# Kernel optimization log

Measured on AMD Instinct MI355X. Metric: run time of the kernel, lower is better.

Reference implementation:

```python
import jax, jax.numpy as jnp
import numpy as np

N_EMBD = 1024
N_HEAD = 16

def setup_inputs() -> dict:
    key = jax.random.key(0)
    ks = jax.random.split(key, 5)
    C = N_EMBD
    x = jax.random.normal(ks[0], (4, 2048, C), dtype=jnp.float32)
    s = 1.0 / np.sqrt(C)
    W_attn = jax.random.normal(ks[1], (C, 3 * C), dtype=jnp.float32) * s
    b_attn = jnp.zeros((3 * C,), dtype=jnp.float32)
    W_proj = jax.random.normal(ks[2], (C, C), dtype=jnp.float32) * s
    b_proj = jnp.zeros((C,), dtype=jnp.float32)
    return {"x": x, "W_attn": W_attn, "b_attn": b_attn, "W_proj": W_proj, "b_proj": b_proj}

def reference(x, W_attn, b_attn, W_proj, b_proj):
    B, S, C = x.shape
    Nh = N_HEAD
    Ne = C // Nh
    qkv = x @ W_attn + b_attn                      # [B,S,3C]
    q, k, v = jnp.split(qkv, 3, axis=-1)
    def heads(t):
        return t.reshape(B, S, Nh, Ne).transpose(0, 2, 1, 3)  # [B,Nh,S,Ne]
    q, k, v = heads(q), heads(k), heads(v)
    scale = 1.0 / np.sqrt(Ne)
    att = scale * jnp.einsum('bhqe,bhke->bhqk', q, k)          # [B,Nh,S,S]
    mask = jnp.tril(jnp.ones((S, S), dtype=bool))
    att = jnp.where(mask, att, -jnp.inf)
    att = jax.nn.softmax(att, axis=-1)
    y = jnp.einsum('bhqk,bhke->bhqe', att, v)                  # [B,Nh,S,Ne]
    y = y.transpose(0, 2, 1, 3).reshape(B, S, C)
    return y @ W_proj + b_proj
```

## Files before the change

### kernel.cpp

```cpp
#include <hip/hip_runtime.h>
#include <cstdint>
#include <cstddef>

typedef _Float16 h16;
typedef _Float16 h16x4 __attribute__((ext_vector_type(4)));
typedef _Float16 h16x8 __attribute__((ext_vector_type(8)));
typedef __fp16 fp16x2 __attribute__((ext_vector_type(2)));
typedef float f32x4 __attribute__((ext_vector_type(4)));

#define LOG2E 1.44269504088896f
#define QSCALE (0.125f * LOG2E)
#define THR 11.0f

static __device__ __forceinline__ f32x4 mfma_f16(h16x8 a, h16x8 b, f32x4 c) {
  return __builtin_amdgcn_mfma_f32_16x16x32_f16(a, b, c, 0, 0, 0);
}

static __device__ __forceinline__ void gload_lds16(const void* g, void* s) {
  __builtin_amdgcn_global_load_lds(
      (__attribute__((address_space(1))) void*)(uintptr_t)g,
      (__attribute__((address_space(3))) void*)s, 16, 0, 0);
}

__global__ __launch_bounds__(256) void k_cvt(const float* __restrict__ in,
                                             h16* __restrict__ out, int n) {
  int i = (blockIdx.x * 256 + threadIdx.x) * 8;
  if (i >= n) return;
  float4 a = *(const float4*)(in + i);
  float4 b = *(const float4*)(in + i + 4);
  h16x8 o;
  o[0] = (h16)a.x; o[1] = (h16)a.y; o[2] = (h16)a.z; o[3] = (h16)a.w;
  o[4] = (h16)b.x; o[5] = (h16)b.y; o[6] = (h16)b.z; o[7] = (h16)b.w;
  *(h16x8*)(out + i) = o;
}

__global__ __launch_bounds__(256) void k_tr_cvt(const float* __restrict__ in,
                                                h16* __restrict__ out, int R, int C) {
  __shared__ float tile[32][33];
  int c0 = blockIdx.x * 32, r0 = blockIdx.y * 32;
  int tx = threadIdx.x & 31, ty = threadIdx.x >> 5;
#pragma unroll
  for (int i = 0; i < 4; i++) {
    int r = ty + i * 8;
    tile[r][tx] = in[(size_t)(r0 + r) * C + c0 + tx];
  }
  __syncthreads();
#pragma unroll
  for (int i = 0; i < 4; i++) {
    int c = ty + i * 8;
    out[(size_t)(c0 + c) * R + r0 + tx] = (h16)tile[tx][c];
  }
}

static __device__ __forceinline__ void gemm_main(const h16* __restrict__ A,
                                                 const h16* __restrict__ BT,
                                                 int K, int m0, int n0,
                                                 h16* sA, h16* sB, f32x4 acc[4][4]) {
  const int t = threadIdx.x;
  const int l = t & 63, w = t >> 6;
  const int lm = l & 15, lh = l >> 4;
  const int wm = (w >> 1) * 64, wn = (w & 1) * 64;

  const h16* gA0 = A + (size_t)(m0 + (t >> 2)) * K + (t & 3) * 8;
  const h16* gB0 = BT + (size_t)(n0 + (t >> 2)) * K + (t & 3) * 8;
  h16* sAw = sA + w * 512;
  h16* sBw = sB + w * 512;

  for (int k0 = 0; k0 < K; k0 += 32) {
    gload_lds16(gA0 + k0, sAw);
    gload_lds16(gA0 + (size_t)64 * K + k0, sAw + 2048);
    gload_lds16(gB0 + k0, sBw);
    gload_lds16(gB0 + (size_t)64 * K + k0, sBw + 2048);
    __syncthreads();
    h16x8 af[4], bfv[4];
#pragma unroll
    for (int mi = 0; mi < 4; mi++)
      af[mi] = *(const h16x8*)(sA + (wm + mi * 16 + lm) * 32 + lh * 8);
#pragma unroll
    for (int ni = 0; ni < 4; ni++)
      bfv[ni] = *(const h16x8*)(sB + (wn + ni * 16 + lm) * 32 + lh * 8);
#pragma unroll
    for (int mi = 0; mi < 4; mi++)
#pragma unroll
      for (int ni = 0; ni < 4; ni++)
        acc[mi][ni] = mfma_f16(af[mi], bfv[ni], acc[mi][ni]);
    __syncthreads();
  }
}

__global__ __launch_bounds__(256) void k_gemm_qkv(const h16* __restrict__ xb,
                                                  const h16* __restrict__ WTa,
                                                  const float* __restrict__ b_attn,
                                                  h16* __restrict__ qb, h16* __restrict__ kbuf,
                                                  h16* __restrict__ vT) {
  __shared__ __align__(16) h16 sA[128 * 32];
  __shared__ __align__(16) h16 sB[128 * 32];
  f32x4 acc[4][4];
#pragma unroll
  for (int i = 0; i < 4; i++)
#pragma unroll
    for (int j = 0; j < 4; j++) acc[i][j] = (f32x4){0.f, 0.f, 0.f, 0.f};
  const int n0 = blockIdx.x * 128, m0 = blockIdx.y * 128;
  gemm_main(xb, WTa, 1024, m0, n0, sA, sB, acc);

  const int t = threadIdx.x, l = t & 63, w = t >> 6;
  const int lm = l & 15, lh = l >> 4;
  const int wm = (w >> 1) * 64, wn = (w & 1) * 64;
#pragma unroll
  for (int mi = 0; mi < 4; mi++) {
#pragma unroll
    for (int ni = 0; ni < 4; ni++) {
      const int n = n0 + wn + ni * 16 + lm;
      const float bias = b_attn[n];
      const int which = n >> 10, c = n & 1023, h = c >> 6, e = c & 63;
#pragma unroll
      for (int r = 0; r < 4; r++) {
        const int m = m0 + wm + mi * 16 + lh * 4 + r;
        const int b = m >> 11, s = m & 2047;
        const h16 o = (h16)(acc[mi][ni][r] + bias);
        const size_t bh = (size_t)(b * 16 + h);
        if (which == 0)      qb[(bh * 2048 + s) * 64 + e] = o;
        else if (which == 1) kbuf[(bh * 2048 + s) * 64 + e] = o;
        else                 vT[(bh * 64 + e) * 2048 + s] = o;
      }
    }
  }
}

__global__ __launch_bounds__(256) void k_gemm_proj(const h16* __restrict__ yb,
                                                   const h16* __restrict__ WTp,
                                                   const float* __restrict__ b_proj,
                                                   float* __restrict__ out) {
  __shared__ __align__(16) h16 sA[128 * 32];
  __shared__ __align__(16) h16 sB[128 * 32];
  f32x4 acc[4][4];
#pragma unroll
  for (int i = 0; i < 4; i++)
#pragma unroll
    for (int j = 0; j < 4; j++) acc[i][j] = (f32x4){0.f, 0.f, 0.f, 0.f};
  const int n0 = blockIdx.x * 128, m0 = blockIdx.y * 128;
  gemm_main(yb, WTp, 1024, m0, n0, sA, sB, acc);

  const int t = threadIdx.x, l = t & 63, w = t >> 6;
  const int lm = l & 15, lh = l >> 4;
  const int wm = (w >> 1) * 64, wn = (w & 1) * 64;
#pragma unroll
  for (int mi = 0; mi < 4; mi++) {
#pragma unroll
    for (int ni = 0; ni < 4; ni++) {
      const int n = n0 + wn + ni * 16 + lm;
      const float bias = b_proj[n];
#pragma unroll
      for (int r = 0; r < 4; r++) {
        const int m = m0 + wm + mi * 16 + lh * 4 + r;
        out[(size_t)m * 1024 + n] = acc[mi][ni][r] + bias;
      }
    }
  }
}

__global__ __launch_bounds__(256, 3) void k_attn(const h16* __restrict__ qb,
                                                 const h16* __restrict__ kbuf,
                                                 const h16* __restrict__ vT,
                                                 h16* __restrict__ yb) {
  __shared__ __align__(16) h16 sKt[2][64 * 64];
  __shared__ __align__(16) h16 sVt[2][64 * 64];
  __shared__ __align__(16) h16 sP[4][2][16 * 64];

  const int bid = blockIdx.x;
  const int bh = bid & 63;
  const int qt = 15 - (bid >> 6);
  const int b = bh >> 4, h = bh & 15;
  const int tid = threadIdx.x, lam = tid & 63, w = tid >> 6;
  const int lm = lam & 15, lh = lam >> 4;
  const int q0 = qt * 128 + w * 32;
  const h16* Q = qb + (size_t)bh * 2048 * 64;
  const h16* Kp = kbuf + (size_t)bh * 2048 * 64;
  const h16* Vp = vT + (size_t)bh * 64 * 2048;

  const int srow = lam >> 3;
  const int xo8 = (((lam & 7) ^ (srow & 7)) << 3);

  h16x8 qf[2][2];
#pragma unroll
  for (int rt = 0; rt < 2; rt++)
#pragma unroll
    for (int dc = 0; dc < 2; dc++) {
      h16x8 qv = *(const h16x8*)(Q + (size_t)(q0 + rt * 16 + lm) * 64 + dc * 32 + lh * 8);
      h16x8 o;
#pragma unroll
      for (int i = 0; i < 8; i++) o[i] = (h16)((float)qv[i] * QSCALE);
      qf[rt][dc] = o;
    }

  f32x4 yacc[2][4];
  float m2[2], lw[2];
#pragma unroll
  for (int rt = 0; rt < 2; rt++) {
    m2[rt] = -1e30f;
    lw[rt] = 0.f;
#pragma unroll
    for (int i = 0; i < 4; i++) yacc[rt][i] = (f32x4){0.f, 0.f, 0.f, 0.f};
  }

  const int nsteps = qt * 2 + 2;

#pragma unroll
  for (int i = 0; i < 2; i++) {
    const int seg = 2 * w + i;
    const int r = seg * 8 + srow;
    gload_lds16(Kp + (size_t)r * 64 + xo8, &sKt[0][seg * 512]);
    gload_lds16(Vp + (size_t)r * 2048 + xo8, &sVt[0][seg * 512]);
  }
  asm volatile("s_waitcnt vmcnt(0)" ::: "memory");
  __syncthreads();

  for (int tt = 0; tt < nsteps; ++tt) {
    const int kb0 = tt * 64, cur = tt & 1;
    if (tt + 1 < nsteps) {
      const int kn = kb0 + 64;
#pragma unroll
      for (int i = 0; i < 2; i++) {
        const int seg = 2 * w + i;
        const int r = seg * 8 + srow;
        gload_lds16(Kp + (size_t)(kn + r) * 64 + xo8, &sKt[cur ^ 1][seg * 512]);
        gload_lds16(Vp + (size_t)r * 2048 + kn + xo8, &sVt[cur ^ 1][seg * 512]);
      }
    }
    if (kb0 <= q0 + 31) {
      const bool domask = (kb0 + 63 > q0);
      h16x8 kf[4][2];
#pragma unroll
      for (int ct = 0; ct < 4; ct++)
#pragma unroll
        for (int dc = 0; dc < 2; dc++)
          kf[ct][dc] = *(const h16x8*)(
              &sKt[cur][(ct * 16 + lm) * 64 + ((dc * 32 + lh * 8) ^ ((lm & 7) << 3))]);
      h16x8 vf[4][2];
#pragma unroll
      for (int dt = 0; dt < 4; dt++)
#pragma unroll
        for (int kc = 0; kc < 2; kc++)
          vf[dt][kc] = *(const h16x8*)(
              &sVt[cur][(dt * 16 + lm) * 64 + ((kc * 32 + lh * 8) ^ ((lm & 7) << 3))]);

#pragma unroll
      for (int rt = 0; rt < 2; rt++) {
        const int qrow = q0 + rt * 16 + lm;
        f32x4 sv[4];
        __builtin_amdgcn_s_setprio(1);
#pragma unroll
        for (int ct = 0; ct < 4; ct++) {
          f32x4 s = mfma_f16(kf[ct][0], qf[rt][0], (f32x4){0.f, 0.f, 0.f, 0.f});
          sv[ct] = mfma_f16(kf[ct][1], qf[rt][1], s);
        }
        __builtin_amdgcn_s_setprio(0);
        if (domask) {
#pragma unroll
          for (int ct = 0; ct < 4; ct++)
#pragma unroll
            for (int r = 0; r < 4; r++)
              if (kb0 + ct * 16 + lh * 4 + r > qrow) sv[ct][r] = -1e30f;
        }
        float rm = fmaxf(fmaxf(fmaxf(sv[0][0], sv[0][1]), fmaxf(sv[0][2], sv[0][3])),
                         fmaxf(fmaxf(sv[1][0], sv[1][1]), fmaxf(sv[1][2], sv[1][3])));
        rm = fmaxf(rm, fmaxf(fmaxf(fmaxf(sv[2][0], sv[2][1]), fmaxf(sv[2][2], sv[2][3])),
                             fmaxf(fmaxf(sv[3][0], sv[3][1]), fmaxf(sv[3][2], sv[3][3]))));
        rm = fmaxf(rm, __shfl_xor(rm, 16));
        rm = fmaxf(rm, __shfl_xor(rm, 32));
        if (!__all(rm <= m2[rt] + THR)) {
          const float nm = fmaxf(m2[rt], rm);
          const float alpha = __builtin_amdgcn_exp2f(m2[rt] - nm);
          m2[rt] = nm;
          lw[rt] *= alpha;
#pragma unroll
          for (int dt = 0; dt < 4; dt++) yacc[rt][dt] *= alpha;
        }
        const float m = m2[rt];
        float psum = 0.f;
#pragma unroll
        for (int ct = 0; ct < 4; ct++) {
          const float p0 = __builtin_amdgcn_exp2f(sv[ct][0] - m);
          const float p1 = __builtin_amdgcn_exp2f(sv[ct][1] - m);
          const float p2 = __builtin_amdgcn_exp2f(sv[ct][2] - m);
          const float p3 = __builtin_amdgcn_exp2f(sv[ct][3] - m);
          psum += (p0 + p1) + (p2 + p3);
          const fp16x2 u0 = __builtin_amdgcn_cvt_pkrtz(p0, p1);
          const fp16x2 u1 = __builtin_amdgcn_cvt_pkrtz(p2, p3);
          const int base = ct * 16 + lh * 4;
          *(fp16x2*)(&sP[w][rt][lm * 64 + ((base + 0) ^ ((lm & 7) << 3))]) = u0;
          *(fp16x2*)(&sP[w][rt][lm * 64 + ((base + 2) ^ ((lm & 7) << 3))]) = u1;
        }
        lw[rt] += psum;
      }
#pragma unroll
      for (int rt = 0; rt < 2; rt++) {
        const h16x8 pf0 = *(const h16x8*)(
            &sP[w][rt][lm * 64 + ((lh * 8) ^ ((lm & 7) << 3))]);
        const h16x8 pf1 = *(const h16x8*)(
            &sP[w][rt][lm * 64 + ((32 + lh * 8) ^ ((lm & 7) << 3))]);
        __builtin_amdgcn_s_setprio(1);
#pragma unroll
        for (int dt = 0; dt < 4; dt++) {
          f32x4 y = mfma_f16(vf[dt][0], pf0, yacc[rt][dt]);
          yacc[rt][dt] = mfma_f16(vf[dt][1], pf1, y);
        }
        __builtin_amdgcn_s_setprio(0);
      }
    }
    asm volatile("s_waitcnt vmcnt(0)" ::: "memory");
    __syncthreads();
  }

#pragma unroll
  for (int rt = 0; rt < 2; rt++) {
    float s = lw[rt];
    s += __shfl_xor(s, 16);
    s += __shfl_xor(s, 32);
    const float inv = 1.0f / s;
    const int q = q0 + rt * 16 + lm;
    const size_t yrow = ((size_t)b * 2048 + q) * 1024 + h * 64;
#pragma unroll
    for (int dt = 0; dt < 4; dt++) {
      h16x4 o;
#pragma unroll
      for (int r = 0; r < 4; r++) o[r] = (h16)(yacc[rt][dt][r] * inv);
      *(h16x4*)(yb + yrow + dt * 16 + lh * 4) = o;
    }
  }
}

extern "C" void kernel_launch(void* const* d_in, const int* in_sizes, int n_in,
                              void* d_out, int out_size, void* d_ws, size_t ws_size,
                              hipStream_t stream) {
  const float* x      = (const float*)d_in[0];
  const float* W_attn = (const float*)d_in[1];
  const float* b_attn = (const float*)d_in[2];
  const float* W_proj = (const float*)d_in[3];
  const float* b_proj = (const float*)d_in[4];
  float* out = (float*)d_out;

  char* ws = (char*)d_ws;
  h16* xb   = (h16*)(ws);
  h16* WTa  = (h16*)(ws + 16777216);
  h16* WTp  = (h16*)(ws + 23068672);
  h16* qb   = (h16*)(ws + 25165824);
  h16* kbuf = (h16*)(ws + 41943040);
  h16* vT   = (h16*)(ws + 58720256);
  h16* yb   = xb;

  k_cvt<<<dim3(8192 * 1024 / 2048), 256, 0, stream>>>(x, xb, 8192 * 1024);
  k_tr_cvt<<<dim3(3072 / 32, 1024 / 32), 256, 0, stream>>>(W_attn, WTa, 1024, 3072);
  k_tr_cvt<<<dim3(1024 / 32, 1024 / 32), 256, 0, stream>>>(W_proj, WTp, 1024, 1024);
  k_gemm_qkv<<<dim3(3072 / 128, 8192 / 128), 256, 0, stream>>>(xb, WTa, b_attn, qb, kbuf, vT);
  k_attn<<<dim3(64 * 16), 256, 0, stream>>>(qb, kbuf, vT, yb);
  k_gemm_proj<<<dim3(1024 / 128, 8192 / 128), 256, 0, stream>>>(yb, WTp, b_proj, out);
}
```

Baseline: 299.5 us.

## Rewrite GEMMs with 256x128 tiles, triple-buffered async LDS loads, swizzle and XCD remap

Both projection GEMMs now use 512-thread blocks on 256x128 tiles with K-step 64. Loads go to a three-slot LDS ring through async global_load_lds, waited on with vmcnt and a single barrier per iteration, so two stages are in flight during compute. LDS columns are XOR-swizzled to avoid bank conflicts, and block IDs are remapped across the 8 XCDs for cache locality. The goal is to hide global latency and remove the two-barrier, single-buffer stalls of the old loop, at the cost of more LDS per block (144KB) and fewer resident blocks.

```diff
diff --git a/kernel.cpp b/kernel.cpp
--- a/kernel.cpp
+++ b/kernel.cpp
@@ -52,73 +52,108 @@
   }
 }
 
-static __device__ __forceinline__ void gemm_main(const h16* __restrict__ A,
-                                                 const h16* __restrict__ BT,
-                                                 int K, int m0, int n0,
-                                                 h16* sA, h16* sB, f32x4 acc[4][4]) {
-  const int t = threadIdx.x;
-  const int l = t & 63, w = t >> 6;
-  const int lm = l & 15, lh = l >> 4;
-  const int wm = (w >> 1) * 64, wn = (w & 1) * 64;
-
-  const h16* gA0 = A + (size_t)(m0 + (t >> 2)) * K + (t & 3) * 8;
-  const h16* gB0 = BT + (size_t)(n0 + (t >> 2)) * K + (t & 3) * 8;
-  h16* sAw = sA + w * 512;
-  h16* sBw = sB + w * 512;
-
-  for (int k0 = 0; k0 < K; k0 += 32) {
-    gload_lds16(gA0 + k0, sAw);
-    gload_lds16(gA0 + (size_t)64 * K + k0, sAw + 2048);
-    gload_lds16(gB0 + k0, sBw);
-    gload_lds16(gB0 + (size_t)64 * K + k0, sBw + 2048);
-    __syncthreads();
-    h16x8 af[4], bfv[4];
+#define SLOT_H16 24576
+#define NT_K 16
+
+static __device__ __forceinline__ void gemm_main256(
+    const h16* __restrict__ A, const h16* __restrict__ BT,
+    int m0, int n0, h16* sAB, f32x4 acc[4][4]) {
+  const int tid = threadIdx.x;
+  const int lane = tid & 63, w = tid >> 6;
+  const int lm = lane & 15, lh = lane >> 4;
+  const int wr = w >> 1, wc = w & 1;
+  const int wbase = w * 512;
+  const int srow = tid >> 3;
+  const int scol = (((tid & 7) ^ (srow & 7)) << 3);
+  const h16* gA = A + (size_t)(m0 + srow) * 1024 + scol;
+  const h16* gB = BT + (size_t)(n0 + srow) * 1024 + scol;
+
+  auto stage = [&](int t, int sl) {
+    const int k = t * 64;
+    h16* d = sAB + sl * SLOT_H16 + wbase;
+    gload_lds16(gA + (size_t)0 * 65536 + k, d + 0 * 4096);
+    gload_lds16(gA + (size_t)1 * 65536 + k, d + 1 * 4096);
+    gload_lds16(gA + (size_t)2 * 65536 + k, d + 2 * 4096);
+    gload_lds16(gA + (size_t)3 * 65536 + k, d + 3 * 4096);
+    gload_lds16(gB + (size_t)0 * 65536 + k, d + 16384 + 0 * 4096);
+    gload_lds16(gB + (size_t)1 * 65536 + k, d + 16384 + 1 * 4096);
+  };
+
+  stage(0, 0);
+  stage(1, 1);
+  asm volatile("s_waitcnt vmcnt(6)" ::: "memory");
+  __builtin_amdgcn_s_barrier();
+
+  int sl = 0, ss = 2;
+  for (int t = 0; t < NT_K; ++t) {
+    if (t < NT_K - 2) stage(t + 2, ss);
+    const h16* sa = sAB + sl * SLOT_H16;
+    const h16* sb = sa + 16384;
+    h16x8 af[4][2], bf[4][2];
+#pragma unroll
+    for (int mi = 0; mi < 4; mi++) {
+      const int row = wr * 64 + mi * 16 + lm;
+#pragma unroll
+      for (int kk = 0; kk < 2; kk++)
+        af[mi][kk] = *(const h16x8*)(sa + row * 64 + ((kk * 32 + lh * 8) ^ ((lm & 7) << 3)));
+    }
+#pragma unroll
+    for (int ni = 0; ni < 4; ni++) {
+      const int row = wc * 64 + ni * 16 + lm;
+#pragma unroll
+      for (int kk = 0; kk < 2; kk++)
+        bf[ni][kk] = *(const h16x8*)(sb + row * 64 + ((kk * 32 + lh * 8) ^ ((lm & 7) << 3)));
+    }
+    __builtin_amdgcn_s_setprio(1);
 #pragma unroll
     for (int mi = 0; mi < 4; mi++)
-      af[mi] = *(const h16x8*)(sA + (wm + mi * 16 + lm) * 32 + lh * 8);
-#pragma unroll
-    for (int ni = 0; ni < 4; ni++)
-      bfv[ni] = *(const h16x8*)(sB + (wn + ni * 16 + lm) * 32 + lh * 8);
-#pragma unroll
-    for (int mi = 0; mi < 4; mi++)
 #pragma unroll
       for (int ni = 0; ni < 4; ni++)
-        acc[mi][ni] = mfma_f16(af[mi], bfv[ni], acc[mi][ni]);
-    __syncthreads();
-  }
-}
-
-__global__ __launch_bounds__(256) void k_gemm_qkv(const h16* __restrict__ xb,
-                                                  const h16* __restrict__ WTa,
-                                                  const float* __restrict__ b_attn,
-                                                  h16* __restrict__ qb, h16* __restrict__ kbuf,
-                                                  h16* __restrict__ vT) {
-  __shared__ __align__(16) h16 sA[128 * 32];
-  __shared__ __align__(16) h16 sB[128 * 32];
+        acc[mi][ni] = mfma_f16(af[mi][1], bf[ni][1],
+                               mfma_f16(af[mi][0], bf[ni][0], acc[mi][ni]));
+    __builtin_amdgcn_s_setprio(0);
+    if (t < NT_K - 2) asm volatile("s_waitcnt vmcnt(6)" ::: "memory");
+    else              asm volatile("s_waitcnt vmcnt(0)" ::: "memory");
+    __builtin_amdgcn_s_barrier();
+    sl = (sl == 2) ? 0 : sl + 1;
+    ss = (ss == 2) ? 0 : ss + 1;
+  }
+}
+
+__global__ __launch_bounds__(512, 2) void k_gemm_qkv(const h16* __restrict__ xb,
+                                                     const h16* __restrict__ WTa,
+                                                     const float* __restrict__ b_attn,
+                                                     h16* __restrict__ qb,
+                                                     h16* __restrict__ kbuf,
+                                                     h16* __restrict__ vT) {
+  __shared__ __align__(16) h16 sAB[3 * SLOT_H16];
+  const int bid = blockIdx.x;
+  const int flat = (bid & 7) * 96 + (bid >> 3);
+  const int mt = flat / 24, nt = flat % 24;
+  const int m0 = mt * 256, n0 = nt * 128;
   f32x4 acc[4][4];
 #pragma unroll
   for (int i = 0; i < 4; i++)
 #pragma unroll
     for (int j = 0; j < 4; j++) acc[i][j] = (f32x4){0.f, 0.f, 0.f, 0.f};
-  const int n0 = blockIdx.x * 128, m0 = blockIdx.y * 128;
-  gemm_main(xb, WTa, 1024, m0, n0, sA, sB, acc);
-
-  const int t = threadIdx.x, l = t & 63, w = t >> 6;
-  const int lm = l & 15, lh = l >> 4;
-  const int wm = (w >> 1) * 64, wn = (w & 1) * 64;
-#pragma unroll
-  for (int mi = 0; mi < 4; mi++) {
-#pragma unroll
-    for (int ni = 0; ni < 4; ni++) {
-      const int n = n0 + wn + ni * 16 + lm;
-      const float bias = b_attn[n];
-      const int which = n >> 10, c = n & 1023, h = c >> 6, e = c & 63;
+  gemm_main256(xb, WTa, m0, n0, sAB, acc);
+
+  const int tid = threadIdx.x, lane = tid & 63, w = tid >> 6;
+  const int lm = lane & 15, lh = lane >> 4;
+  const int wr = w >> 1, wc = w & 1;
+#pragma unroll
+  for (int ni = 0; ni < 4; ni++) {
+    const int n = n0 + wc * 64 + ni * 16 + lm;
+    const float bias = b_attn[n];
+    const int which = n >> 10, cc = n & 1023, hh = cc >> 6, e = cc & 63;
+#pragma unroll
+    for (int mi = 0; mi < 4; mi++) {
 #pragma unroll
       for (int r = 0; r < 4; r++) {
-        const int m = m0 + wm + mi * 16 + lh * 4 + r;
+        const int m = m0 + wr * 64 + mi * 16 + lh * 4 + r;
         const int b = m >> 11, s = m & 2047;
         const h16 o = (h16)(acc[mi][ni][r] + bias);
-        const size_t bh = (size_t)(b * 16 + h);
+        const size_t bh = (size_t)(b * 16 + hh);
         if (which == 0)      qb[(bh * 2048 + s) * 64 + e] = o;
         else if (which == 1) kbuf[(bh * 2048 + s) * 64 + e] = o;
         else                 vT[(bh * 64 + e) * 2048 + s] = o;
@@ -127,32 +162,34 @@
   }
 }
 
-__global__ __launch_bounds__(256) void k_gemm_proj(const h16* __restrict__ yb,
-                                                   const h16* __restrict__ WTp,
-                                                   const float* __restrict__ b_proj,
-                                                   float* __restrict__ out) {
-  __shared__ __align__(16) h16 sA[128 * 32];
-  __shared__ __align__(16) h16 sB[128 * 32];
+__global__ __launch_bounds__(512, 2) void k_gemm_proj(const h16* __restrict__ yb,
+                                                      const h16* __restrict__ WTp,
+                                                      const float* __restrict__ b_proj,
+                                                      float* __restrict__ out) {
+  __shared__ __align__(16) h16 sAB[3 * SLOT_H16];
+  const int bid = blockIdx.x;
+  const int flat = (bid & 7) * 32 + (bid >> 3);
+  const int mt = flat / 8, nt = flat % 8;
+  const int m0 = mt * 256, n0 = nt * 128;
   f32x4 acc[4][4];
 #pragma unroll
   for (int i = 0; i < 4; i++)
 #pragma unroll
     for (int j = 0; j < 4; j++) acc[i][j] = (f32x4){0.f, 0.f, 0.f, 0.f};
-  const int n0 = blockIdx.x * 128, m0 = blockIdx.y * 128;
-  gemm_main(yb, WTp, 1024, m0, n0, sA, sB, acc);
-
-  const int t = threadIdx.x, l = t & 63, w = t >> 6;
-  const int lm = l & 15, lh = l >> 4;
-  const int wm = (w >> 1) * 64, wn = (w & 1) * 64;
-#pragma unroll
-  for (int mi = 0; mi < 4; mi++) {
-#pragma unroll
-    for (int ni = 0; ni < 4; ni++) {
-      const int n = n0 + wn + ni * 16 + lm;
-      const float bias = b_proj[n];
+  gemm_main256(yb, WTp, m0, n0, sAB, acc);
+
+  const int tid = threadIdx.x, lane = tid & 63, w = tid >> 6;
+  const int lm = lane & 15, lh = lane >> 4;
+  const int wr = w >> 1, wc = w & 1;
+#pragma unroll
+  for (int ni = 0; ni < 4; ni++) {
+    const int n = n0 + wc * 64 + ni * 16 + lm;
+    const float bias = b_proj[n];
+#pragma unroll
+    for (int mi = 0; mi < 4; mi++) {
 #pragma unroll
       for (int r = 0; r < 4; r++) {
-        const int m = m0 + wm + mi * 16 + lh * 4 + r;
+        const int m = m0 + wr * 64 + mi * 16 + lh * 4 + r;
         out[(size_t)m * 1024 + n] = acc[mi][ni][r] + bias;
       }
     }
@@ -352,7 +389,7 @@
   k_cvt<<<dim3(8192 * 1024 / 2048), 256, 0, stream>>>(x, xb, 8192 * 1024);
   k_tr_cvt<<<dim3(3072 / 32, 1024 / 32), 256, 0, stream>>>(W_attn, WTa, 1024, 3072);
   k_tr_cvt<<<dim3(1024 / 32, 1024 / 32), 256, 0, stream>>>(W_proj, WTp, 1024, 1024);
-  k_gemm_qkv<<<dim3(3072 / 128, 8192 / 128), 256, 0, stream>>>(xb, WTa, b_attn, qb, kbuf, vT);
+  k_gemm_qkv<<<dim3(768), 512, 0, stream>>>(xb, WTa, b_attn, qb, kbuf, vT);
   k_attn<<<dim3(64 * 16), 256, 0, stream>>>(qb, kbuf, vT, yb);
-  k_gemm_proj<<<dim3(1024 / 128, 8192 / 128), 256, 0, stream>>>(yb, WTp, b_proj, out);
-}
+  k_gemm_proj<<<dim3(256), 512, 0, stream>>>(yb, WTp, b_proj, out);
+}
```

Result: faster. 290.9 us (-2.9%).

## Load attention K/V fragments directly from global and swizzle GEMM LDS tiles

Applied to the files above, without the earlier changes.

The attention kernel no longer stages K and V tiles in double-buffered shared memory with block-wide barriers. Each wave now loads its K and V MFMA fragments straight from global memory, and each wave iterates only over the key blocks it needs, with no block synchronisation. This removes LDS traffic and the __syncthreads per step, but every wave loads the same K/V from global or L2 separately, and there is no explicit prefetch to hide latency. Separately, the GEMM LDS layout gets an XOR swizzle on the 16-byte chunks to reduce bank conflicts on the fragment reads.

```diff
diff --git a/kernel.cpp b/kernel.cpp
--- a/kernel.cpp
+++ b/kernel.cpp
@@ -61,10 +61,14 @@
   const int lm = l & 15, lh = l >> 4;
   const int wm = (w >> 1) * 64, wn = (w & 1) * 64;
 
-  const h16* gA0 = A + (size_t)(m0 + (t >> 2)) * K + (t & 3) * 8;
-  const h16* gB0 = BT + (size_t)(n0 + (t >> 2)) * K + (t & 3) * 8;
+  const int srow = t >> 2;
+  const int schunk = (t & 3) ^ ((srow >> 1) & 3);
+  const h16* gA0 = A + (size_t)(m0 + srow) * K + schunk * 8;
+  const h16* gB0 = BT + (size_t)(n0 + srow) * K + schunk * 8;
   h16* sAw = sA + w * 512;
   h16* sBw = sB + w * 512;
+
+  const int swa = ((lm >> 1) & 3);
 
   for (int k0 = 0; k0 < K; k0 += 32) {
     gload_lds16(gA0 + k0, sAw);
@@ -75,10 +79,10 @@
     h16x8 af[4], bfv[4];
 #pragma unroll
     for (int mi = 0; mi < 4; mi++)
-      af[mi] = *(const h16x8*)(sA + (wm + mi * 16 + lm) * 32 + lh * 8);
+      af[mi] = *(const h16x8*)(sA + (wm + mi * 16 + lm) * 32 + ((lh ^ swa) << 3));
 #pragma unroll
     for (int ni = 0; ni < 4; ni++)
-      bfv[ni] = *(const h16x8*)(sB + (wn + ni * 16 + lm) * 32 + lh * 8);
+      bfv[ni] = *(const h16x8*)(sB + (wn + ni * 16 + lm) * 32 + ((lh ^ swa) << 3));
 #pragma unroll
     for (int mi = 0; mi < 4; mi++)
 #pragma unroll
@@ -163,8 +167,6 @@
                                                  const h16* __restrict__ kbuf,
                                                  const h16* __restrict__ vT,
                                                  h16* __restrict__ yb) {
-  __shared__ __align__(16) h16 sKt[2][64 * 64];
-  __shared__ __align__(16) h16 sVt[2][64 * 64];
   __shared__ __align__(16) h16 sP[4][2][16 * 64];
 
   const int bid = blockIdx.x;
@@ -178,9 +180,6 @@
   const h16* Kp = kbuf + (size_t)bh * 2048 * 64;
   const h16* Vp = vT + (size_t)bh * 64 * 2048;
 
-  const int srow = lam >> 3;
-  const int xo8 = (((lam & 7) ^ (srow & 7)) << 3);
-
   h16x8 qf[2][2];
 #pragma unroll
   for (int rt = 0; rt < 2; rt++)
@@ -203,113 +202,86 @@
     for (int i = 0; i < 4; i++) yacc[rt][i] = (f32x4){0.f, 0.f, 0.f, 0.f};
   }
 
-  const int nsteps = qt * 2 + 2;
-
-#pragma unroll
-  for (int i = 0; i < 2; i++) {
-    const int seg = 2 * w + i;
-    const int r = seg * 8 + srow;
-    gload_lds16(Kp + (size_t)r * 64 + xo8, &sKt[0][seg * 512]);
-    gload_lds16(Vp + (size_t)r * 2048 + xo8, &sVt[0][seg * 512]);
-  }
-  asm volatile("s_waitcnt vmcnt(0)" ::: "memory");
-  __syncthreads();
-
-  for (int tt = 0; tt < nsteps; ++tt) {
-    const int kb0 = tt * 64, cur = tt & 1;
-    if (tt + 1 < nsteps) {
-      const int kn = kb0 + 64;
-#pragma unroll
-      for (int i = 0; i < 2; i++) {
-        const int seg = 2 * w + i;
-        const int r = seg * 8 + srow;
-        gload_lds16(Kp + (size_t)(kn + r) * 64 + xo8, &sKt[cur ^ 1][seg * 512]);
-        gload_lds16(Vp + (size_t)r * 2048 + kn + xo8, &sVt[cur ^ 1][seg * 512]);
-      }
-    }
-    if (kb0 <= q0 + 31) {
-      const bool domask = (kb0 + 63 > q0);
-      h16x8 kf[4][2];
-#pragma unroll
-      for (int ct = 0; ct < 4; ct++)
-#pragma unroll
-        for (int dc = 0; dc < 2; dc++)
-          kf[ct][dc] = *(const h16x8*)(
-              &sKt[cur][(ct * 16 + lm) * 64 + ((dc * 32 + lh * 8) ^ ((lm & 7) << 3))]);
-      h16x8 vf[4][2];
-#pragma unroll
-      for (int dt = 0; dt < 4; dt++)
-#pragma unroll
-        for (int kc = 0; kc < 2; kc++)
-          vf[dt][kc] = *(const h16x8*)(
-              &sVt[cur][(dt * 16 + lm) * 64 + ((kc * 32 + lh * 8) ^ ((lm & 7) << 3))]);
-
-#pragma unroll
-      for (int rt = 0; rt < 2; rt++) {
-        const int qrow = q0 + rt * 16 + lm;
-        f32x4 sv[4];
-        __builtin_amdgcn_s_setprio(1);
-#pragma unroll
-        for (int ct = 0; ct < 4; ct++) {
-          f32x4 s = mfma_f16(kf[ct][0], qf[rt][0], (f32x4){0.f, 0.f, 0.f, 0.f});
-          sv[ct] = mfma_f16(kf[ct][1], qf[rt][1], s);
-        }
-        __builtin_amdgcn_s_setprio(0);
-        if (domask) {
-#pragma unroll
-          for (int ct = 0; ct < 4; ct++)
-#pragma unroll
-            for (int r = 0; r < 4; r++)
-              if (kb0 + ct * 16 + lh * 4 + r > qrow) sv[ct][r] = -1e30f;
-        }
-        float rm = fmaxf(fmaxf(fmaxf(sv[0][0], sv[0][1]), fmaxf(sv[0][2], sv[0][3])),
-                         fmaxf(fmaxf(sv[1][0], sv[1][1]), fmaxf(sv[1][2], sv[1][3])));
-        rm = fmaxf(rm, fmaxf(fmaxf(fmaxf(sv[2][0], sv[2][1]), fmaxf(sv[2][2], sv[2][3])),
-                             fmaxf(fmaxf(sv[3][0], sv[3][1]), fmaxf(sv[3][2], sv[3][3]))));
-        rm = fmaxf(rm, __shfl_xor(rm, 16));
-        rm = fmaxf(rm, __shfl_xor(rm, 32));
-        if (!__all(rm <= m2[rt] + THR)) {
-          const float nm = fmaxf(m2[rt], rm);
-          const float alpha = __builtin_amdgcn_exp2f(m2[rt] - nm);
-          m2[rt] = nm;
-          lw[rt] *= alpha;
-#pragma unroll
-          for (int dt = 0; dt < 4; dt++) yacc[rt][dt] *= alpha;
-        }
-        const float m = m2[rt];
-        float psum = 0.f;
-#pragma unroll
-        for (int ct = 0; ct < 4; ct++) {
-          const float p0 = __builtin_amdgcn_exp2f(sv[ct][0] - m);
-          const float p1 = __builtin_amdgcn_exp2f(sv[ct][1] - m);
-          const float p2 = __builtin_amdgcn_exp2f(sv[ct][2] - m);
-          const float p3 = __builtin_amdgcn_exp2f(sv[ct][3] - m);
-          psum += (p0 + p1) + (p2 + p3);
-          const fp16x2 u0 = __builtin_amdgcn_cvt_pkrtz(p0, p1);
-          const fp16x2 u1 = __builtin_amdgcn_cvt_pkrtz(p2, p3);
-          const int base = ct * 16 + lh * 4;
-          *(fp16x2*)(&sP[w][rt][lm * 64 + ((base + 0) ^ ((lm & 7) << 3))]) = u0;
-          *(fp16x2*)(&sP[w][rt][lm * 64 + ((base + 2) ^ ((lm & 7) << 3))]) = u1;
-        }
-        lw[rt] += psum;
-      }
-#pragma unroll
-      for (int rt = 0; rt < 2; rt++) {
-        const h16x8 pf0 = *(const h16x8*)(
-            &sP[w][rt][lm * 64 + ((lh * 8) ^ ((lm & 7) << 3))]);
-        const h16x8 pf1 = *(const h16x8*)(
-            &sP[w][rt][lm * 64 + ((32 + lh * 8) ^ ((lm & 7) << 3))]);
-        __builtin_amdgcn_s_setprio(1);
-#pragma unroll
-        for (int dt = 0; dt < 4; dt++) {
-          f32x4 y = mfma_f16(vf[dt][0], pf0, yacc[rt][dt]);
-          yacc[rt][dt] = mfma_f16(vf[dt][1], pf1, y);
-        }
-        __builtin_amdgcn_s_setprio(0);
-      }
-    }
-    asm volatile("s_waitcnt vmcnt(0)" ::: "memory");
-    __syncthreads();
+  for (int kb0 = 0; kb0 <= q0 + 31; kb0 += 64) {
+    const bool domask = (kb0 + 63 > q0);
+    h16x8 kf[4][2];
+#pragma unroll
+    for (int ct = 0; ct < 4; ct++)
+#pragma unroll
+      for (int dc = 0; dc < 2; dc++)
+        kf[ct][dc] = *(const h16x8*)(Kp + (size_t)(kb0 + ct * 16 + lm) * 64 + dc * 32 + lh * 8);
+    h16x8 vf[4][2];
+#pragma unroll
+    for (int dt = 0; dt < 4; dt++)
+#pragma unroll
+      for (int kc = 0; kc < 2; kc++)
+        vf[dt][kc] = *(const h16x8*)(Vp + (size_t)(dt * 16 + lm) * 2048 + kb0 + kc * 32 + lh * 8);
+
+#pragma unroll
+    for (int rt = 0; rt < 2; rt++) {
+      const int qrow = q0 + rt * 16 + lm;
+      f32x4 sv[4];
+      __builtin_amdgcn_s_setprio(1);
+#pragma unroll
+      for (int ct = 0; ct < 4; ct++) {
+        f32x4 s = mfma_f16(kf[ct][0], qf[rt][0], (f32x4){0.f, 0.f, 0.f, 0.f});
+        sv[ct] = mfma_f16(kf[ct][1], qf[rt][1], s);
+      }
+      __builtin_amdgcn_s_setprio(0);
+      if (domask) {
+#pragma unroll
+        for (int ct = 0; ct < 4; ct++)
+#pragma unroll
+          for (int r = 0; r < 4; r++)
+            if (kb0 + ct * 16 + lh * 4 + r > qrow) sv[ct][r] = -1e30f;
+      }
+      float rm = fmaxf(fmaxf(fmaxf(sv[0][0], sv[0][1]), fmaxf(sv[0][2], sv[0][3])),
+                       fmaxf(fmaxf(sv[1][0], sv[1][1]), fmaxf(sv[1][2], sv[1][3])));
+      rm = fmaxf(rm, fmaxf(fmaxf(fmaxf(sv[2][0], sv[2][1]), fmaxf(sv[2][2], sv[2][3])),
+                           fmaxf(fmaxf(sv[3][0], sv[3][1]), fmaxf(sv[3][2], sv[3][3]))));
+      rm = fmaxf(rm, __shfl_xor(rm, 16));
+      rm = fmaxf(rm, __shfl_xor(rm, 32));
+      if (!__all(rm <= m2[rt] + THR)) {
+        const float nm = fmaxf(m2[rt], rm);
+        const float alpha = __builtin_amdgcn_exp2f(m2[rt] - nm);
+        m2[rt] = nm;
+        lw[rt] *= alpha;
+#pragma unroll
+        for (int dt = 0; dt < 4; dt++) yacc[rt][dt] *= alpha;
+      }
+      const float m = m2[rt];
+      float psum = 0.f;
+#pragma unroll
+      for (int ct = 0; ct < 4; ct++) {
+        const float p0 = __builtin_amdgcn_exp2f(sv[ct][0] - m);
+        const float p1 = __builtin_amdgcn_exp2f(sv[ct][1] - m);
+        const float p2 = __builtin_amdgcn_exp2f(sv[ct][2] - m);
+        const float p3 = __builtin_amdgcn_exp2f(sv[ct][3] - m);
+        psum += (p0 + p1) + (p2 + p3);
+        const fp16x2 u0 = __builtin_amdgcn_cvt_pkrtz(p0, p1);
+        const fp16x2 u1 = __builtin_amdgcn_cvt_pkrtz(p2, p3);
+        const int base = ct * 16 + lh * 4;
+        *(fp16x2*)(&sP[w][rt][lm * 64 + ((base + 0) ^ ((lm & 7) << 3))]) = u0;
+        *(fp16x2*)(&sP[w][rt][lm * 64 + ((base + 2) ^ ((lm & 7) << 3))]) = u1;
+      }
+      lw[rt] += psum;
+    }
+    asm volatile("s_waitcnt lgkmcnt(0)" ::: "memory");
+    __builtin_amdgcn_sched_barrier(0);
+#pragma unroll
+    for (int rt = 0; rt < 2; rt++) {
+      const h16x8 pf0 = *(const h16x8*)(
+          &sP[w][rt][lm * 64 + ((lh * 8) ^ ((lm & 7) << 3))]);
+      const h16x8 pf1 = *(const h16x8*)(
+          &sP[w][rt][lm * 64 + ((32 + lh * 8) ^ ((lm & 7) << 3))]);
+      __builtin_amdgcn_s_setprio(1);
+#pragma unroll
+      for (int dt = 0; dt < 4; dt++) {
+        f32x4 y = mfma_f16(vf[dt][0], pf0, yacc[rt][dt]);
+        yacc[rt][dt] = mfma_f16(vf[dt][1], pf1, y);
+      }
+      __builtin_amdgcn_s_setprio(0);
+    }
   }
 
 #pragma unroll
```

Result: slower. 371.2 us (+24.0%).
